# Performance work log

Measured on AMD Instinct MI355X. Metric: run time of the kernel, lower is better.

## Reference

```python
import jax, jax.numpy as jnp
import numpy as np

N_ITERS = 150   # unrolled projected-subgradient iterations of the convex DRO program
LR0 = 0.05      # initial step size (decays as 1/sqrt(k))


def project_simplex(v):
    """Euclidean projection of v onto the probability simplex {z >= 0, sum z = 1}."""
    n = v.shape[0]
    u = jnp.sort(v)[::-1]
    css = jnp.cumsum(u)
    idx = jnp.arange(1, n + 1, dtype=v.dtype)
    rho = jnp.sum(u + (1.0 - css) / idx > 0)
    theta = (css[rho - 1] - 1.0) / rho.astype(v.dtype)
    return jnp.maximum(v - theta, 0.0)


def dro_solve(ep, y_hat, delta, gamma):
    """Solve the TV-DRO portfolio problem (Ben-Tal et al. 2013 tractable dual):
        min_{z in simplex, c, eta, lam>=0}
            eta + delta*lam + (1/T) sum_t max(-lam, (ep_t@z - c)^2 - eta) - gamma * y_hat@z
    via unrolled projected subgradient descent (differentiable solver layer).
    """
    n_obs, n_y = ep.shape

    def objective(params):
        z, c, eta, lam = params
        r = ep @ z - c                       # (n_obs,) residual portfolio returns
        m = jnp.maximum(-lam, r * r - eta)   # TV phi-conjugate term
        return eta + delta * lam + jnp.mean(m) - gamma * jnp.dot(y_hat, z)

    grad_fn = jax.grad(objective)
    init = (jnp.full((n_y,), 1.0 / n_y, dtype=ep.dtype),
            jnp.zeros((), ep.dtype), jnp.zeros((), ep.dtype),
            jnp.asarray(0.1, ep.dtype))

    def step(params, k):
        g = grad_fn(params)
        lr = LR0 / jnp.sqrt(1.0 + k)
        z, c, eta, lam = [p - lr * gi for p, gi in zip(params, g)]
        z = project_simplex(z)
        lam = jnp.maximum(lam, 0.0)
        return (z, c, eta, lam), None

    (z, _, _, _), _ = jax.lax.scan(step, init, jnp.arange(N_ITERS, dtype=ep.dtype))
    return z


def setup_inputs() -> dict:
    key = jax.random.key(0)
    k1, k2, k3, k4 = jax.random.split(key, 4)
    n_obs, n_x, n_y = 256, 64, 128
    X = jax.random.normal(k1, (n_obs, n_x), dtype=jnp.float32)
    Y = 0.05 * jax.random.normal(k2, (n_obs, n_y), dtype=jnp.float32)
    W = jax.random.normal(k3, (n_y, n_x), dtype=jnp.float32) / np.sqrt(n_x)
    b = 0.01 * jax.random.normal(k4, (n_y,), dtype=jnp.float32)
    delta = jnp.asarray(0.1, jnp.float32)
    gamma = jnp.asarray(0.1, jnp.float32)
    return {"X": X, "Y": Y, "W": W, "b": b, "delta": delta, "gamma": gamma}


def reference(X, Y, W, b, delta, gamma):
    Y_hat = X @ W.T + b            # pred_layer applied to each x_t (batched)
    ep = Y - Y_hat                 # (n_obs, n_y) residuals
    # One DRO solve per scenario y_hat_t, all sharing the same residual matrix ep.
    Z_star = jax.vmap(lambda yh: dro_solve(ep, yh, delta, gamma))(Y_hat)
    return Z_star, Y_hat
```

## Files before the change

kernel.cpp:

```cpp
#include <hip/hip_runtime.h>
#include <math.h>

#define T_OBS 256
#define NY 128
#define NITER 150

#define DPP_ROW_SHR1 0x111
#define DPP_ROW_SHR2 0x112
#define DPP_ROW_SHR4 0x114
#define DPP_ROW_SHR8 0x118
#define DPP_BCAST15  0x142
#define DPP_BCAST31  0x143

#define DPP_ADD_F32(x, ctrl) \
    (x) += __int_as_float(__builtin_amdgcn_update_dpp(0, __float_as_int(x), (ctrl), 0xf, 0xf, true))

__device__ __forceinline__ void wave_sum2(float& a, float& b) {
    DPP_ADD_F32(a, DPP_ROW_SHR1); DPP_ADD_F32(b, DPP_ROW_SHR1);
    DPP_ADD_F32(a, DPP_ROW_SHR2); DPP_ADD_F32(b, DPP_ROW_SHR2);
    DPP_ADD_F32(a, DPP_ROW_SHR4); DPP_ADD_F32(b, DPP_ROW_SHR4);
    DPP_ADD_F32(a, DPP_ROW_SHR8); DPP_ADD_F32(b, DPP_ROW_SHR8);
    DPP_ADD_F32(a, DPP_BCAST15);  DPP_ADD_F32(b, DPP_BCAST15);
    DPP_ADD_F32(a, DPP_BCAST31);  DPP_ADD_F32(b, DPP_BCAST31);
    a = __int_as_float(__builtin_amdgcn_readlane(__float_as_int(a), 63));
    b = __int_as_float(__builtin_amdgcn_readlane(__float_as_int(b), 63));
}

__device__ __forceinline__ float rl(float x, int l) {
    return __int_as_float(__builtin_amdgcn_readlane(__float_as_int(x), l));
}

__global__ __launch_bounds__(128)
void pred_kernel(const float* __restrict__ X, const float* __restrict__ Y,
                 const float* __restrict__ W, const float* __restrict__ b,
                 float* __restrict__ yhat, float* __restrict__ ep) {
    __shared__ float xrow[64];
    const int t = blockIdx.x;
    const int j = threadIdx.x;
    if (j < 64) xrow[j] = X[t * 64 + j];
    __syncthreads();
    const float* wr = W + j * 64;
    float acc = 0.f;
#pragma unroll
    for (int x = 0; x < 64; ++x) acc = fmaf(xrow[x], wr[x], acc);
    const float yh = acc + b[j];
    yhat[t * NY + j] = yh;
    ep[t * NY + j] = Y[t * NY + j] - yh;
}

__global__ __launch_bounds__(256, 1)
void dro_kernel(const float* __restrict__ ep_g, const float* __restrict__ yhat_g,
                float* __restrict__ z_out,
                const float* __restrict__ d_delta, const float* __restrict__ d_gamma) {
    __shared__ float gzp[2][4][NY];
    __shared__ __align__(16) float red[2][8];

    const int tid  = threadIdx.x;
    const int lane = tid & 63;
    const int wid  = tid >> 6;
    const int blk  = blockIdx.x;

    float4 rA[32];
    {
        const float4* eg4 = (const float4*)ep_g + tid * 32;
#pragma unroll
        for (int q = 0; q < 32; ++q) rA[q] = eg4[q];
    }

    const int j0    = lane << 1;
    const int tbase = wid << 6;
    float2 rB[64];
#pragma unroll
    for (int tt = 0; tt < 64; ++tt)
        rB[tt] = *(const float2*)(ep_g + (tbase + tt) * NY + j0);

    const float yh0 = yhat_g[blk * NY + j0];
    const float yh1 = yhat_g[blk * NY + j0 + 1];

    float z0 = 1.0f / 128.0f, z1 = 1.0f / 128.0f;
    float act0 = 1.f, act1 = 1.f;

    const float delta = d_delta[0];
    const float gamma = d_gamma[0];
    float c = 0.f, eta = 0.f, lam = 0.1f;
    int buf = 0;

    for (int k = 0; k < NITER; ++k) {
        const float lr = 0.05f * __builtin_amdgcn_rsqf(1.0f + (float)k);

        float a0 = 0.f, a1 = 0.f, a2 = 0.f, a3 = 0.f;
#pragma unroll
        for (int q = 0; q < 32; ++q) {
            const float4 e = rA[q];
            const float za = rl(z0, 2 * q);
            const float zb = rl(z1, 2 * q);
            const float zc = rl(z0, 2 * q + 1);
            const float zd = rl(z1, 2 * q + 1);
            a0 = fmaf(e.x, za, a0);
            a1 = fmaf(e.y, zb, a1);
            a2 = fmaf(e.z, zc, a2);
            a3 = fmaf(e.w, zd, a3);
        }
        const float r  = (a0 + a1) + (a2 + a3) - c;
        const float q2 = r * r - eta;
        const float aa = -lam;
        const float st = (q2 > aa) ? 1.0f : ((q2 == aa) ? 0.5f : 0.0f);
        const float wv = st * r;

        float s1 = st, s2 = wv;
        wave_sum2(s1, s2);
        if (lane == 0) { red[buf][wid * 2] = s1; red[buf][wid * 2 + 1] = s2; }

        float p0 = 0.f, p1 = 0.f, p2 = 0.f, p3 = 0.f;
#pragma unroll
        for (int tt = 0; tt < 64; tt += 2) {
            const float wa = rl(wv, tt);
            const float wb = rl(wv, tt + 1);
            const float2 ea = rB[tt];
            const float2 eb = rB[tt + 1];
            p0 = fmaf(wa, ea.x, p0);
            p1 = fmaf(wa, ea.y, p1);
            p2 = fmaf(wb, eb.x, p2);
            p3 = fmaf(wb, eb.y, p3);
        }
        *(float2*)&gzp[buf][wid][j0] = make_float2(p0 + p2, p1 + p3);

        __syncthreads();

        const float4 rd0 = *(const float4*)&red[buf][0];
        const float4 rd1 = *(const float4*)&red[buf][4];
        const float S1 = (rd0.x + rd0.z) + (rd1.x + rd1.z);
        const float S2 = (rd0.y + rd0.w) + (rd1.y + rd1.w);
        c   -= lr * (-(2.0f / 256.0f) * S2);
        eta -= lr * (1.0f - S1 * (1.0f / 256.0f));
        lam  = fmaxf(lam - lr * (delta - 1.0f + S1 * (1.0f / 256.0f)), 0.0f);

        const float2 g0v = *(const float2*)&gzp[buf][0][j0];
        const float2 g1v = *(const float2*)&gzp[buf][1][j0];
        const float2 g2v = *(const float2*)&gzp[buf][2][j0];
        const float2 g3v = *(const float2*)&gzp[buf][3][j0];
        const float g0 = (g0v.x + g1v.x) + (g2v.x + g3v.x);
        const float g1 = (g0v.y + g1v.y) + (g2v.y + g3v.y);
        const float v0 = z0 - lr * ((2.0f / 256.0f) * g0 - gamma * yh0);
        const float v1 = z1 - lr * ((2.0f / 256.0f) * g1 - gamma * yh1);

        float theta = 0.f;
        for (int attempt = 0; attempt < 2; ++attempt) {
            for (int m = 0; m < 128; ++m) {
                float s  = act0 * v0 + act1 * v1;
                float cc = act0 + act1;
                wave_sum2(s, cc);
                theta = (s - 1.0f) * __builtin_amdgcn_rcpf(cc);
                const float n0 = (v0 > theta) ? act0 : 0.f;
                const float n1 = (v1 > theta) ? act1 : 0.f;
                const bool changed = (n0 != act0) || (n1 != act1);
                act0 = n0; act1 = n1;
                if (!__any(changed)) break;
            }
            const bool viol = ((act0 == 0.f) && (v0 > theta)) ||
                              ((act1 == 0.f) && (v1 > theta));
            if (!__any(viol)) break;
            act0 = 1.f; act1 = 1.f;
        }
        z0 = fmaxf(v0 - theta, 0.f);
        z1 = fmaxf(v1 - theta, 0.f);

        buf ^= 1;
    }

    if (wid == 0) *(float2*)&z_out[blk * NY + j0] = make_float2(z0, z1);
}

extern "C" void kernel_launch(void* const* d_in, const int* in_sizes, int n_in,
                              void* d_out, int out_size, void* d_ws, size_t ws_size,
                              hipStream_t stream) {
    const float* X       = (const float*)d_in[0];
    const float* Y       = (const float*)d_in[1];
    const float* W       = (const float*)d_in[2];
    const float* b       = (const float*)d_in[3];
    const float* d_delta = (const float*)d_in[4];
    const float* d_gamma = (const float*)d_in[5];

    float* z_out    = (float*)d_out;
    float* yhat_out = z_out + T_OBS * NY;
    float* ep_ws    = (float*)d_ws;

    pred_kernel<<<T_OBS, 128, 0, stream>>>(X, Y, W, b, yhat_out, ep_ws);
    dro_kernel<<<T_OBS, 256, 0, stream>>>(ep_ws, yhat_out, z_out, d_delta, d_gamma);
}
```

Measured before the change: 238.0 us.

## Store residual matrix in fp16 and use packed dot2 for both matvecs

The residual matrix is now written in fp16, once row-major and once as column pairs packed in a transposed layout. The dro kernel keeps it in half-width registers and computes both matvecs with v_dot2 on packed half2 operands. This halves the readlane broadcasts and the FMA count per iteration and cuts register pressure. In exchange, z, the subgradient weights and the residuals are rounded to fp16, which adds error to the gradients and to the simplex projection and could push results past tolerance.

```diff
diff --git a/kernel.cpp b/kernel.cpp
--- a/kernel.cpp
+++ b/kernel.cpp
@@ -4,6 +4,8 @@
 #define T_OBS 256
 #define NY 128
 #define NITER 150
+
+typedef __fp16 half2_t __attribute__((ext_vector_type(2)));
 
 #define DPP_ROW_SHR1 0x111
 #define DPP_ROW_SHR2 0x112
@@ -11,6 +13,7 @@
 #define DPP_ROW_SHR8 0x118
 #define DPP_BCAST15  0x142
 #define DPP_BCAST31  0x143
+#define DPP_QUAD_X1  0xB1
 
 #define DPP_ADD_F32(x, ctrl) \
     (x) += __int_as_float(__builtin_amdgcn_update_dpp(0, __float_as_int(x), (ctrl), 0xf, 0xf, true))
@@ -26,31 +29,57 @@
     b = __int_as_float(__builtin_amdgcn_readlane(__float_as_int(b), 63));
 }
 
-__device__ __forceinline__ float rl(float x, int l) {
-    return __int_as_float(__builtin_amdgcn_readlane(__float_as_int(x), l));
+__device__ __forceinline__ unsigned rlu(unsigned x, int l) {
+    return (unsigned)__builtin_amdgcn_readlane((int)x, l);
+}
+__device__ __forceinline__ unsigned h2u(half2_t h) {
+    return __builtin_bit_cast(unsigned, h);
+}
+__device__ __forceinline__ half2_t u2h(unsigned u) {
+    return __builtin_bit_cast(half2_t, u);
+}
+__device__ __forceinline__ float dot2u(unsigned a, unsigned b, float c) {
+#if __has_builtin(__builtin_amdgcn_fdot2)
+    return __builtin_amdgcn_fdot2(u2h(a), u2h(b), c, false);
+#else
+    half2_t ha = u2h(a), hb = u2h(b);
+    return fmaf((float)ha.y, (float)hb.y, fmaf((float)ha.x, (float)hb.x, c));
+#endif
 }
 
 __global__ __launch_bounds__(128)
 void pred_kernel(const float* __restrict__ X, const float* __restrict__ Y,
-                 const float* __restrict__ W, const float* __restrict__ b,
-                 float* __restrict__ yhat, float* __restrict__ ep) {
-    __shared__ float xrow[64];
-    const int t = blockIdx.x;
-    const int j = threadIdx.x;
-    if (j < 64) xrow[j] = X[t * 64 + j];
+                 const float* __restrict__ W, const float* __restrict__ bb,
+                 float* __restrict__ yhat, __fp16* __restrict__ ep_row,
+                 unsigned* __restrict__ ep_cp) {
+    __shared__ float xrow[128];
+    const int blk = blockIdx.x;
+    const int j   = threadIdx.x;
+    const int t0  = blk << 1;
+    xrow[j] = X[t0 * 64 + j];
     __syncthreads();
     const float* wr = W + j * 64;
-    float acc = 0.f;
-#pragma unroll
-    for (int x = 0; x < 64; ++x) acc = fmaf(xrow[x], wr[x], acc);
-    const float yh = acc + b[j];
-    yhat[t * NY + j] = yh;
-    ep[t * NY + j] = Y[t * NY + j] - yh;
+    float a0 = 0.f, a1 = 0.f;
+#pragma unroll
+    for (int x = 0; x < 64; ++x) {
+        const float w = wr[x];
+        a0 = fmaf(xrow[x],      w, a0);
+        a1 = fmaf(xrow[64 + x], w, a1);
+    }
+    const float yh0 = a0 + bb[j];
+    const float yh1 = a1 + bb[j];
+    yhat[t0 * NY + j]       = yh0;
+    yhat[(t0 + 1) * NY + j] = yh1;
+    const float e0 = Y[t0 * NY + j] - yh0;
+    const float e1 = Y[(t0 + 1) * NY + j] - yh1;
+    ep_row[t0 * NY + j]       = (__fp16)e0;
+    ep_row[(t0 + 1) * NY + j] = (__fp16)e1;
+    ep_cp[j * 128 + blk] = h2u(__builtin_amdgcn_cvt_pkrtz(e0, e1));
 }
 
 __global__ __launch_bounds__(256, 1)
-void dro_kernel(const float* __restrict__ ep_g, const float* __restrict__ yhat_g,
-                float* __restrict__ z_out,
+void dro_kernel(const __fp16* __restrict__ ep_row, const unsigned* __restrict__ ep_cp,
+                const float* __restrict__ yhat_g, float* __restrict__ z_out,
                 const float* __restrict__ d_delta, const float* __restrict__ d_gamma) {
     __shared__ float gzp[2][4][NY];
     __shared__ __align__(16) float red[2][8];
@@ -60,19 +89,26 @@
     const int wid  = tid >> 6;
     const int blk  = blockIdx.x;
 
-    float4 rA[32];
+    unsigned rA[64];
     {
-        const float4* eg4 = (const float4*)ep_g + tid * 32;
-#pragma unroll
-        for (int q = 0; q < 32; ++q) rA[q] = eg4[q];
+        const uint4* p = (const uint4*)(ep_row + tid * NY);
+#pragma unroll
+        for (int q = 0; q < 16; ++q) {
+            const uint4 v = p[q];
+            rA[4 * q + 0] = v.x; rA[4 * q + 1] = v.y;
+            rA[4 * q + 2] = v.z; rA[4 * q + 3] = v.w;
+        }
     }
 
     const int j0    = lane << 1;
     const int tbase = wid << 6;
-    float2 rB[64];
-#pragma unroll
-    for (int tt = 0; tt < 64; ++tt)
-        rB[tt] = *(const float2*)(ep_g + (tbase + tt) * NY + j0);
+    unsigned rb0[32], rb1[32];
+    {
+        const unsigned* c0 = ep_cp + j0 * 128 + (tbase >> 1);
+        const unsigned* c1 = ep_cp + (j0 + 1) * 128 + (tbase >> 1);
+#pragma unroll
+        for (int i = 0; i < 32; ++i) { rb0[i] = c0[i]; rb1[i] = c1[i]; }
+    }
 
     const float yh0 = yhat_g[blk * NY + j0];
     const float yh1 = yhat_g[blk * NY + j0 + 1];
@@ -88,20 +124,14 @@
     for (int k = 0; k < NITER; ++k) {
         const float lr = 0.05f * __builtin_amdgcn_rsqf(1.0f + (float)k);
 
-        float a0 = 0.f, a1 = 0.f, a2 = 0.f, a3 = 0.f;
-#pragma unroll
-        for (int q = 0; q < 32; ++q) {
-            const float4 e = rA[q];
-            const float za = rl(z0, 2 * q);
-            const float zb = rl(z1, 2 * q);
-            const float zc = rl(z0, 2 * q + 1);
-            const float zd = rl(z1, 2 * q + 1);
-            a0 = fmaf(e.x, za, a0);
-            a1 = fmaf(e.y, zb, a1);
-            a2 = fmaf(e.z, zc, a2);
-            a3 = fmaf(e.w, zd, a3);
-        }
-        const float r  = (a0 + a1) + (a2 + a3) - c;
+        const unsigned zp = h2u(__builtin_amdgcn_cvt_pkrtz(z0, z1));
+        float acA = 0.f, acB = 0.f;
+#pragma unroll
+        for (int q = 0; q < 64; q += 2) {
+            acA = dot2u(rA[q],     rlu(zp, q),     acA);
+            acB = dot2u(rA[q + 1], rlu(zp, q + 1), acB);
+        }
+        const float r  = acA + acB - c;
         const float q2 = r * r - eta;
         const float aa = -lam;
         const float st = (q2 > aa) ? 1.0f : ((q2 == aa) ? 0.5f : 0.0f);
@@ -111,19 +141,18 @@
         wave_sum2(s1, s2);
         if (lane == 0) { red[buf][wid * 2] = s1; red[buf][wid * 2 + 1] = s2; }
 
-        float p0 = 0.f, p1 = 0.f, p2 = 0.f, p3 = 0.f;
-#pragma unroll
-        for (int tt = 0; tt < 64; tt += 2) {
-            const float wa = rl(wv, tt);
-            const float wb = rl(wv, tt + 1);
-            const float2 ea = rB[tt];
-            const float2 eb = rB[tt + 1];
-            p0 = fmaf(wa, ea.x, p0);
-            p1 = fmaf(wa, ea.y, p1);
-            p2 = fmaf(wb, eb.x, p2);
-            p3 = fmaf(wb, eb.y, p3);
-        }
-        *(float2*)&gzp[buf][wid][j0] = make_float2(p0 + p2, p1 + p3);
+        const float wpart = __int_as_float(
+            __builtin_amdgcn_update_dpp(0, __float_as_int(wv), DPP_QUAD_X1, 0xf, 0xf, true));
+        const unsigned wpk = h2u(__builtin_amdgcn_cvt_pkrtz(wv, wpart));
+
+        float p0 = 0.f, p1 = 0.f;
+#pragma unroll
+        for (int i = 0; i < 32; ++i) {
+            const unsigned wu = rlu(wpk, 2 * i);
+            p0 = dot2u(rb0[i], wu, p0);
+            p1 = dot2u(rb1[i], wu, p1);
+        }
+        *(float2*)&gzp[buf][wid][j0] = make_float2(p0, p1);
 
         __syncthreads();
 
@@ -183,8 +212,10 @@
 
     float* z_out    = (float*)d_out;
     float* yhat_out = z_out + T_OBS * NY;
-    float* ep_ws    = (float*)d_ws;
-
-    pred_kernel<<<T_OBS, 128, 0, stream>>>(X, Y, W, b, yhat_out, ep_ws);
-    dro_kernel<<<T_OBS, 256, 0, stream>>>(ep_ws, yhat_out, z_out, d_delta, d_gamma);
-}
+
+    __fp16*   ep_row = (__fp16*)d_ws;
+    unsigned* ep_cp  = (unsigned*)((char*)d_ws + 65536);
+
+    pred_kernel<<<T_OBS / 2, 128, 0, stream>>>(X, Y, W, b, yhat_out, ep_row, ep_cp);
+    dro_kernel<<<T_OBS, 256, 0, stream>>>(ep_row, ep_cp, yhat_out, z_out, d_delta, d_gamma);
+}
```

Measured after the change: 252.5 us. 6.1% more time.
